# Performance work log

Hardware: AMD Instinct MI355X
Metric: run time of the kernel (lower is better)

## Reference

```python
import jax, jax.numpy as jnp
import numpy as np

EPS = 1e-5
H, I, E = 1024, 2048, 8


def _swiglu(x, wg, wu, wd):
    # x: [T,H], wg/wu: [H,I], wd: [I,H]
    return (jax.nn.silu(x @ wg) * (x @ wu)) @ wd


def setup_inputs() -> dict:
    key = jax.random.key(0)
    ks = jax.random.split(key, 12)
    B, S = 2, 2048
    s_h = 1.0 / np.sqrt(H)
    s_i = 1.0 / np.sqrt(I)
    return {
        "x": jax.random.normal(ks[0], (B, S, H), jnp.float32),
        "temporal_context": jax.random.normal(ks[1], (B, S, H), jnp.float32),
        "tp_w": jax.random.normal(ks[2], (H, H), jnp.float32) * s_h,
        "tp_b": jnp.zeros((H,), jnp.float32),
        "gate_w": jax.random.normal(ks[3], (H, E), jnp.float32) * 0.01,
        "eg": jax.random.normal(ks[4], (E, H, I), jnp.float32) * s_h,
        "eu": jax.random.normal(ks[5], (E, H, I), jnp.float32) * s_h,
        "ed": jax.random.normal(ks[6], (E, I, H), jnp.float32) * s_i,
        "sg": jax.random.normal(ks[7], (H, I), jnp.float32) * s_h,
        "su": jax.random.normal(ks[8], (H, I), jnp.float32) * s_h,
        "sd": jax.random.normal(ks[9], (I, H), jnp.float32) * s_i,
        "top_k": 2,
    }


def reference(x, temporal_context, tp_w, tp_b, gate_w, eg, eu, ed, sg, su, sd, top_k):
    B, S, Hd = x.shape
    xf = x.reshape(-1, Hd)                      # [T,H] tokens
    tc = temporal_context.reshape(-1, Hd)
    # Router: add temporal projection, softmax gate, top-k renormalized
    xr = xf + tc @ tp_w + tp_b
    probs = jax.nn.softmax(xr @ gate_w, axis=-1)            # [T,E]
    topk_p, topk_i = jax.lax.top_k(probs, top_k)            # [T,K]
    topk_p = topk_p / (topk_p.sum(-1, keepdims=True) + EPS)
    # Dense combine weights: combine[t,e] = sum_k topk_p[t,k] * 1[topk_i[t,k]==e]
    combine = jnp.einsum("tke,tk->te", jax.nn.one_hot(topk_i, E, dtype=x.dtype), topk_p)
    # Expert SwiGLU (grouped GEMM over all experts)
    h = jax.nn.silu(jnp.einsum("th,ehi->tei", xf, eg)) * jnp.einsum("th,ehi->tei", xf, eu)
    eout = jnp.einsum("tei,eih->teh", h, ed)                # [T,E,H]
    out = jnp.einsum("te,teh->th", combine, eout)
    # Shared expert applied to every token
    out = out + _swiglu(xf, sg, su, sd)
    return out.reshape(B, S, Hd)
```

## Files before the change

### kernel.cpp

```cpp
#include <hip/hip_runtime.h>
#include <hip/hip_bf16.h>
#include <stdint.h>

#define HDIM 1024
#define IDIM 2048
#define NEXP 8
#define NEXP1 9
#define TTOK 4096
#define REPS 1e-5f

typedef __bf16 bf16_t;
typedef __bf16 bf16x8 __attribute__((ext_vector_type(8)));
typedef __bf16 bf16x4 __attribute__((ext_vector_type(4)));
typedef float f32x4 __attribute__((ext_vector_type(4)));

__global__ __launch_bounds__(256) void k_convert(const float* __restrict__ src,
                                                 bf16_t* __restrict__ dst) {
    size_t i = ((size_t)blockIdx.x * 256 + threadIdx.x) * 4;
    float4 v = *(const float4*)(src + i);
    bf16x4 o = {(__bf16)v.x, (__bf16)v.y, (__bf16)v.z, (__bf16)v.w};
    *(bf16x4*)(dst + i) = o;
}

__global__ __launch_bounds__(256) void k_transpose(const float* __restrict__ src,
                                                   bf16_t* __restrict__ dst, int R, int C) {
    __shared__ float tile[32][33];
    size_t mat = (size_t)blockIdx.z * (size_t)R * (size_t)C;
    src += mat;
    dst += mat;
    int c0 = blockIdx.x * 32, r0 = blockIdx.y * 32;
    int tx = threadIdx.x, ty = threadIdx.y;
    for (int i = ty; i < 32; i += 8)
        tile[i][tx] = src[(size_t)(r0 + i) * C + c0 + tx];
    __syncthreads();
    for (int i = ty; i < 32; i += 8)
        dst[(size_t)(c0 + i) * R + r0 + tx] = (bf16_t)tile[tx][i];
}

__global__ __launch_bounds__(256) void k_router_prep(const float* __restrict__ tp_w,
                                                     const float* __restrict__ tp_b,
                                                     const float* __restrict__ gw,
                                                     float* __restrict__ A_r,
                                                     float* __restrict__ bg) {
    int idx = blockIdx.x * 256 + threadIdx.x;
    if (idx < HDIM * NEXP) {
        int h = idx >> 3, e = idx & 7;
        const float* wr = tp_w + (size_t)h * HDIM;
        float acc = 0.f;
        for (int j = 0; j < HDIM; j++) acc = fmaf(wr[j], gw[j * NEXP + e], acc);
        A_r[idx] = acc;
    } else if (idx < HDIM * NEXP + NEXP) {
        int e = idx - HDIM * NEXP;
        float acc = 0.f;
        for (int j = 0; j < HDIM; j++) acc = fmaf(tp_b[j], gw[j * NEXP + e], acc);
        bg[e] = acc;
    }
}

__global__ __launch_bounds__(256) void k_router(const float* __restrict__ x,
                                                const float* __restrict__ tcx,
                                                const float* __restrict__ gw,
                                                const float* __restrict__ A_r,
                                                const float* __restrict__ bg,
                                                int* __restrict__ cnt, int* __restrict__ tok,
                                                float* __restrict__ wl, int* __restrict__ sl) {
    int wave = threadIdx.x >> 6, lane = threadIdx.x & 63;
    int t = blockIdx.x * 4 + wave;
    const float* xr = x + (size_t)t * HDIM;
    const float* tr = tcx + (size_t)t * HDIM;
    float lg[NEXP];
    for (int e = 0; e < NEXP; e++) lg[e] = 0.f;
    for (int h = lane; h < HDIM; h += 64) {
        float xv = xr[h], tv = tr[h];
        const float4* g4 = (const float4*)(gw + h * NEXP);
        const float4* a4 = (const float4*)(A_r + h * NEXP);
        float4 g0 = g4[0], g1 = g4[1], a0 = a4[0], a1 = a4[1];
        lg[0] += xv * g0.x + tv * a0.x;
        lg[1] += xv * g0.y + tv * a0.y;
        lg[2] += xv * g0.z + tv * a0.z;
        lg[3] += xv * g0.w + tv * a0.w;
        lg[4] += xv * g1.x + tv * a1.x;
        lg[5] += xv * g1.y + tv * a1.y;
        lg[6] += xv * g1.z + tv * a1.z;
        lg[7] += xv * g1.w + tv * a1.w;
    }
    for (int off = 32; off > 0; off >>= 1)
        for (int e = 0; e < NEXP; e++) lg[e] += __shfl_xor(lg[e], off);
    if (lane == 0) {
        float m = -1e30f;
        for (int e = 0; e < NEXP; e++) {
            lg[e] += bg[e];
            m = fmaxf(m, lg[e]);
        }
        float p[NEXP], Z = 0.f;
        for (int e = 0; e < NEXP; e++) {
            p[e] = __expf(lg[e] - m);
            Z += p[e];
        }
        for (int e = 0; e < NEXP; e++) p[e] /= Z;
        int i1 = 0;
        float b1 = p[0];
        for (int e = 1; e < NEXP; e++)
            if (p[e] > b1) { b1 = p[e]; i1 = e; }
        int i2 = -1;
        float b2 = -1.f;
        for (int e = 0; e < NEXP; e++) {
            if (e == i1) continue;
            if (p[e] > b2) { b2 = p[e]; i2 = e; }
        }
        float s = b1 + b2 + REPS;
        float w1 = b1 / s, w2 = b2 / s;
        int p1 = atomicAdd(&cnt[i1], 1);
        tok[i1 * TTOK + p1] = t;
        wl[i1 * TTOK + p1] = w1;
        sl[i1 * TTOK + p1] = 2 * t;
        int p2 = atomicAdd(&cnt[i2], 1);
        tok[i2 * TTOK + p2] = t;
        wl[i2 * TTOK + p2] = w2;
        sl[i2 * TTOK + p2] = 2 * t + 1;
    }
}

__global__ __launch_bounds__(256) void k_fill_shared(int* __restrict__ cnt, int* __restrict__ tok,
                                                     float* __restrict__ wl, int* __restrict__ sl) {
    int t = blockIdx.x * 256 + threadIdx.x;
    tok[NEXP * TTOK + t] = t;
    wl[NEXP * TTOK + t] = 1.f;
    sl[NEXP * TTOK + t] = 2 * TTOK + t;
    if (t == 0) cnt[NEXP] = TTOK;
}

__global__ __launch_bounds__(256, 2) void k_gateup(const bf16_t* __restrict__ Xb,
                                                   const bf16_t* __restrict__ WgT,
                                                   const bf16_t* __restrict__ WuT,
                                                   bf16_t* __restrict__ Hout,
                                                   const int* __restrict__ tok_l,
                                                   const float* __restrict__ w_l,
                                                   const int* __restrict__ slot_l,
                                                   const int* __restrict__ cnt) {
    int e = blockIdx.z;
    int rows = cnt[e];
    int m0 = blockIdx.y * 128;
    if (m0 >= rows) return;
    int n0 = blockIdx.x * 64;
    const bf16_t* Wg = WgT + (size_t)e * IDIM * HDIM;
    const bf16_t* Wu = WuT + (size_t)e * IDIM * HDIM;
    const int* tl = tok_l + e * TTOK;
    const float* wlp = w_l + e * TTOK;
    const int* sl = slot_l + e * TTOK;

    __shared__ bf16_t As[128][72];
    __shared__ bf16_t Bg[64][72];
    __shared__ bf16_t Bu[64][72];

    int tid = threadIdx.x;
    int lane = tid & 63, wave = tid >> 6;
    int seg = tid & 7, rbase = tid >> 3;

    const bf16_t* aptr[4];
    for (int p = 0; p < 4; p++) {
        int g = m0 + p * 32 + rbase;
        int row = tl[min(g, rows - 1)];
        aptr[p] = Xb + (size_t)row * HDIM + seg * 8;
    }
    const bf16_t* gptr[2];
    const bf16_t* uptr[2];
    for (int p = 0; p < 2; p++) {
        int r = n0 + p * 32 + rbase;
        gptr[p] = Wg + (size_t)r * HDIM + seg * 8;
        uptr[p] = Wu + (size_t)r * HDIM + seg * 8;
    }

    f32x4 accg[2][4], accu[2][4];
    for (int a = 0; a < 2; a++)
        for (int b = 0; b < 4; b++) {
            accg[a][b] = (f32x4){0.f, 0.f, 0.f, 0.f};
            accu[a][b] = (f32x4){0.f, 0.f, 0.f, 0.f};
        }
    int lm = lane & 15, quad = lane >> 4;

    for (int k0 = 0; k0 < HDIM; k0 += 64) {
        for (int p = 0; p < 4; p++)
            *(bf16x8*)&As[p * 32 + rbase][seg * 8] = *(const bf16x8*)(aptr[p] + k0);
        for (int p = 0; p < 2; p++) {
            *(bf16x8*)&Bg[p * 32 + rbase][seg * 8] = *(const bf16x8*)(gptr[p] + k0);
            *(bf16x8*)&Bu[p * 32 + rbase][seg * 8] = *(const bf16x8*)(uptr[p] + k0);
        }
        __syncthreads();
        for (int kk = 0; kk < 2; kk++) {
            bf16x8 af[2], bgf[4], buf_[4];
            for (int mi = 0; mi < 2; mi++)
                af[mi] = *(const bf16x8*)&As[wave * 32 + mi * 16 + lm][kk * 32 + quad * 8];
            for (int ni = 0; ni < 4; ni++) {
                bgf[ni] = *(const bf16x8*)&Bg[ni * 16 + lm][kk * 32 + quad * 8];
                buf_[ni] = *(const bf16x8*)&Bu[ni * 16 + lm][kk * 32 + quad * 8];
            }
            for (int mi = 0; mi < 2; mi++)
                for (int ni = 0; ni < 4; ni++) {
                    accg[mi][ni] = __builtin_amdgcn_mfma_f32_16x16x32_bf16(af[mi], bgf[ni],
                                                                           accg[mi][ni], 0, 0, 0);
                    accu[mi][ni] = __builtin_amdgcn_mfma_f32_16x16x32_bf16(af[mi], buf_[ni],
                                                                           accu[mi][ni], 0, 0, 0);
                }
        }
        __syncthreads();
    }
    for (int mi = 0; mi < 2; mi++)
        for (int j = 0; j < 4; j++) {
            int r = m0 + wave * 32 + mi * 16 + quad * 4 + j;
            if (r >= rows) continue;
            int srow = sl[r];
            float w = wlp[r];
            bf16_t* hp = Hout + (size_t)srow * IDIM + n0 + lm;
            for (int ni = 0; ni < 4; ni++) {
                float g = accg[mi][ni][j];
                float u = accu[mi][ni][j];
                hp[ni * 16] = (bf16_t)(g / (1.f + __expf(-g)) * u * w);
            }
        }
}

__global__ __launch_bounds__(256, 2) void k_down(const bf16_t* __restrict__ Hin,
                                                 const bf16_t* __restrict__ WdT,
                                                 bf16_t* __restrict__ Eout,
                                                 const int* __restrict__ slot_l,
                                                 const int* __restrict__ cnt) {
    int e = blockIdx.z;
    int rows = cnt[e];
    int m0 = blockIdx.y * 128;
    if (m0 >= rows) return;
    int n0 = blockIdx.x * 128;
    const bf16_t* Wd = WdT + (size_t)e * HDIM * IDIM;
    const int* sl = slot_l + e * TTOK;

    __shared__ bf16_t As[128][72];
    __shared__ bf16_t Bs[128][72];

    int tid = threadIdx.x, lane = tid & 63, wave = tid >> 6;
    int seg = tid & 7, rbase = tid >> 3;
    const bf16_t* aptr[4];
    const bf16_t* bptr[4];
    for (int p = 0; p < 4; p++) {
        int g = m0 + p * 32 + rbase;
        int row = sl[min(g, rows - 1)];
        aptr[p] = Hin + (size_t)row * IDIM + seg * 8;
        bptr[p] = Wd + (size_t)(n0 + p * 32 + rbase) * IDIM + seg * 8;
    }
    f32x4 acc[4][4];
    for (int a = 0; a < 4; a++)
        for (int b = 0; b < 4; b++) acc[a][b] = (f32x4){0.f, 0.f, 0.f, 0.f};
    int wm = wave >> 1, wn = wave & 1;
    int lm = lane & 15, quad = lane >> 4;

    for (int k0 = 0; k0 < IDIM; k0 += 64) {
        for (int p = 0; p < 4; p++) {
            *(bf16x8*)&As[p * 32 + rbase][seg * 8] = *(const bf16x8*)(aptr[p] + k0);
            *(bf16x8*)&Bs[p * 32 + rbase][seg * 8] = *(const bf16x8*)(bptr[p] + k0);
        }
        __syncthreads();
        for (int kk = 0; kk < 2; kk++) {
            bf16x8 af[4], bf_[4];
            for (int mi = 0; mi < 4; mi++)
                af[mi] = *(const bf16x8*)&As[wm * 64 + mi * 16 + lm][kk * 32 + quad * 8];
            for (int ni = 0; ni < 4; ni++)
                bf_[ni] = *(const bf16x8*)&Bs[wn * 64 + ni * 16 + lm][kk * 32 + quad * 8];
            for (int mi = 0; mi < 4; mi++)
                for (int ni = 0; ni < 4; ni++)
                    acc[mi][ni] = __builtin_amdgcn_mfma_f32_16x16x32_bf16(af[mi], bf_[ni],
                                                                          acc[mi][ni], 0, 0, 0);
        }
        __syncthreads();
    }
    for (int mi = 0; mi < 4; mi++)
        for (int j = 0; j < 4; j++) {
            int r = m0 + wm * 64 + mi * 16 + quad * 4 + j;
            if (r >= rows) continue;
            int srow = sl[r];
            bf16_t* op = Eout + (size_t)srow * HDIM + n0 + wn * 64 + lm;
            for (int ni = 0; ni < 4; ni++) op[ni * 16] = (bf16_t)acc[mi][ni][j];
        }
}

__global__ __launch_bounds__(256) void k_combine(const bf16_t* __restrict__ Eout,
                                                 float* __restrict__ Out) {
    size_t i = ((size_t)blockIdx.x * 256 + threadIdx.x) * 8;
    size_t t = i / HDIM, h = i % HDIM;
    bf16x8 a = *(const bf16x8*)(Eout + (2 * t) * HDIM + h);
    bf16x8 b = *(const bf16x8*)(Eout + (2 * t + 1) * HDIM + h);
    bf16x8 c = *(const bf16x8*)(Eout + (size_t)(2 * TTOK + t) * HDIM + h);
    float* op = Out + i;
    for (int j = 0; j < 8; j++) op[j] = (float)a[j] + (float)b[j] + (float)c[j];
}

extern "C" void kernel_launch(void* const* d_in, const int* in_sizes, int n_in,
                              void* d_out, int out_size, void* d_ws, size_t ws_size,
                              hipStream_t stream) {
    const float* x = (const float*)d_in[0];
    const float* tcx = (const float*)d_in[1];
    const float* tp_w = (const float*)d_in[2];
    const float* tp_b = (const float*)d_in[3];
    const float* gate_w = (const float*)d_in[4];
    const float* eg = (const float*)d_in[5];
    const float* eu = (const float*)d_in[6];
    const float* ed = (const float*)d_in[7];
    const float* sg = (const float*)d_in[8];
    const float* su = (const float*)d_in[9];
    const float* sd = (const float*)d_in[10];
    float* out = (float*)d_out;

    char* wsp = (char*)d_ws;
    size_t off = 0;
    auto alloc = [&](size_t b) -> void* {
        void* p = wsp + off;
        off += (b + 255) & ~(size_t)255;
        return p;
    };
    bf16_t* xb = (bf16_t*)alloc((size_t)TTOK * HDIM * 2);
    bf16_t* WgT = (bf16_t*)alloc((size_t)NEXP1 * IDIM * HDIM * 2);
    bf16_t* WuT = (bf16_t*)alloc((size_t)NEXP1 * IDIM * HDIM * 2);
    bf16_t* WdT = (bf16_t*)alloc((size_t)NEXP1 * HDIM * IDIM * 2);
    float* A_r = (float*)alloc(HDIM * NEXP * 4);
    float* bg = (float*)alloc(NEXP * 4);
    int* cnt = (int*)alloc(NEXP1 * 4);
    int* tok = (int*)alloc(NEXP1 * TTOK * 4);
    float* wl = (float*)alloc(NEXP1 * TTOK * 4);
    int* sl = (int*)alloc(NEXP1 * TTOK * 4);
    bf16_t* hbuf = (bf16_t*)alloc((size_t)3 * TTOK * IDIM * 2);
    bf16_t* eout = (bf16_t*)alloc((size_t)3 * TTOK * HDIM * 2);

    hipMemsetAsync(cnt, 0, NEXP1 * 4, stream);
    k_convert<<<TTOK * HDIM / 1024, 256, 0, stream>>>(x, xb);
    dim3 tb(32, 8);
    k_transpose<<<dim3(IDIM / 32, HDIM / 32, NEXP), tb, 0, stream>>>(eg, WgT, HDIM, IDIM);
    k_transpose<<<dim3(IDIM / 32, HDIM / 32, NEXP), tb, 0, stream>>>(eu, WuT, HDIM, IDIM);
    k_transpose<<<dim3(HDIM / 32, IDIM / 32, NEXP), tb, 0, stream>>>(ed, WdT, IDIM, HDIM);
    k_transpose<<<dim3(IDIM / 32, HDIM / 32, 1), tb, 0, stream>>>(
        sg, WgT + (size_t)NEXP * IDIM * HDIM, HDIM, IDIM);
    k_transpose<<<dim3(IDIM / 32, HDIM / 32, 1), tb, 0, stream>>>(
        su, WuT + (size_t)NEXP * IDIM * HDIM, HDIM, IDIM);
    k_transpose<<<dim3(HDIM / 32, IDIM / 32, 1), tb, 0, stream>>>(
        sd, WdT + (size_t)NEXP * HDIM * IDIM, IDIM, HDIM);
    k_router_prep<<<33, 256, 0, stream>>>(tp_w, tp_b, gate_w, A_r, bg);
    k_router<<<TTOK / 4, 256, 0, stream>>>(x, tcx, gate_w, A_r, bg, cnt, tok, wl, sl);
    k_fill_shared<<<TTOK / 256, 256, 0, stream>>>(cnt, tok, wl, sl);
    k_gateup<<<dim3(IDIM / 64, TTOK / 128, NEXP1), 256, 0, stream>>>(xb, WgT, WuT, hbuf, tok, wl,
                                                                     sl, cnt);
    k_down<<<dim3(HDIM / 128, TTOK / 128, NEXP1), 256, 0, stream>>>(hbuf, WdT, eout, sl, cnt);
    k_combine<<<TTOK * HDIM / 2048, 256, 0, stream>>>(eout, out);
    (void)in_sizes; (void)n_in; (void)out_size; (void)ws_size;
}
```

Measured before the change: 720.0 us.

## Use direct global-to-LDS loads with XOR swizzle; widen weight transpose tiles

```diff
diff --git a/kernel.cpp b/kernel.cpp
--- a/kernel.cpp
+++ b/kernel.cpp
@@ -14,6 +14,12 @@
 typedef __bf16 bf16x4 __attribute__((ext_vector_type(4)));
 typedef float f32x4 __attribute__((ext_vector_type(4)));
 
+__device__ __forceinline__ void gl_lds16(const bf16_t* g, bf16_t* l) {
+    __builtin_amdgcn_global_load_lds(
+        (const __attribute__((address_space(1))) void*)g,
+        (__attribute__((address_space(3))) void*)l, 16, 0, 0);
+}
+
 __global__ __launch_bounds__(256) void k_convert(const float* __restrict__ src,
                                                  bf16_t* __restrict__ dst) {
     size_t i = ((size_t)blockIdx.x * 256 + threadIdx.x) * 4;
@@ -22,19 +28,27 @@
     *(bf16x4*)(dst + i) = o;
 }
 
-__global__ __launch_bounds__(256) void k_transpose(const float* __restrict__ src,
-                                                   bf16_t* __restrict__ dst, int R, int C) {
-    __shared__ float tile[32][33];
+__global__ __launch_bounds__(256) void k_transpose64(const float* __restrict__ src,
+                                                     bf16_t* __restrict__ dst, int R, int C) {
+    __shared__ float tile[64][65];
     size_t mat = (size_t)blockIdx.z * (size_t)R * (size_t)C;
-    src += mat;
-    dst += mat;
-    int c0 = blockIdx.x * 32, r0 = blockIdx.y * 32;
-    int tx = threadIdx.x, ty = threadIdx.y;
-    for (int i = ty; i < 32; i += 8)
-        tile[i][tx] = src[(size_t)(r0 + i) * C + c0 + tx];
+    int c0 = blockIdx.x * 64, r0 = blockIdx.y * 64;
+    int tid = threadIdx.x;
+    int rr = tid >> 4, cc = (tid & 15) * 4;
+    for (int i = 0; i < 4; i++) {
+        float4 v = *(const float4*)(src + mat + (size_t)(r0 + rr + i * 16) * C + c0 + cc);
+        tile[rr + i * 16][cc + 0] = v.x;
+        tile[rr + i * 16][cc + 1] = v.y;
+        tile[rr + i * 16][cc + 2] = v.z;
+        tile[rr + i * 16][cc + 3] = v.w;
+    }
     __syncthreads();
-    for (int i = ty; i < 32; i += 8)
-        dst[(size_t)(c0 + i) * R + r0 + tx] = (bf16_t)tile[tx][i];
+    int c = tid >> 2, s = (tid & 3) * 16;
+    bf16_t tmp[16];
+    for (int i = 0; i < 16; i++) tmp[i] = (bf16_t)tile[s + i][c];
+    bf16_t* op = dst + mat + (size_t)(c0 + c) * R + r0 + s;
+    *(bf16x8*)op = *(bf16x8*)tmp;
+    *(bf16x8*)(op + 8) = *(bf16x8*)(tmp + 8);
 }
 
 __global__ __launch_bounds__(256) void k_router_prep(const float* __restrict__ tp_w,
@@ -149,26 +163,27 @@
     const float* wlp = w_l + e * TTOK;
     const int* sl = slot_l + e * TTOK;
 
-    __shared__ bf16_t As[128][72];
-    __shared__ bf16_t Bg[64][72];
-    __shared__ bf16_t Bu[64][72];
+    __shared__ __align__(16) bf16_t As[128 * 64];
+    __shared__ __align__(16) bf16_t Bg[64 * 64];
+    __shared__ __align__(16) bf16_t Bu[64 * 64];
 
     int tid = threadIdx.x;
     int lane = tid & 63, wave = tid >> 6;
-    int seg = tid & 7, rbase = tid >> 3;
-
-    const bf16_t* aptr[4];
-    for (int p = 0; p < 4; p++) {
-        int g = m0 + p * 32 + rbase;
-        int row = tl[min(g, rows - 1)];
-        aptr[p] = Xb + (size_t)row * HDIM + seg * 8;
-    }
-    const bf16_t* gptr[2];
-    const bf16_t* uptr[2];
-    for (int p = 0; p < 2; p++) {
-        int r = n0 + p * 32 + rbase;
-        gptr[p] = Wg + (size_t)r * HDIM + seg * 8;
-        uptr[p] = Wu + (size_t)r * HDIM + seg * 8;
+    int lrow = lane >> 3;
+    int lchunk = (lane & 7) ^ lrow;
+
+    const bf16_t* asrc[4];
+    for (int j = 0; j < 4; j++) {
+        int r = (wave * 4 + j) * 8 + lrow;
+        int row = tl[min(m0 + r, rows - 1)];
+        asrc[j] = Xb + (size_t)row * HDIM + lchunk * 8;
+    }
+    const bf16_t* gsrc[2];
+    const bf16_t* usrc[2];
+    for (int j = 0; j < 2; j++) {
+        int r = (wave * 2 + j) * 8 + lrow;
+        gsrc[j] = Wg + (size_t)(n0 + r) * HDIM + lchunk * 8;
+        usrc[j] = Wu + (size_t)(n0 + r) * HDIM + lchunk * 8;
     }
 
     f32x4 accg[2][4], accu[2][4];
@@ -177,23 +192,23 @@
             accg[a][b] = (f32x4){0.f, 0.f, 0.f, 0.f};
             accu[a][b] = (f32x4){0.f, 0.f, 0.f, 0.f};
         }
-    int lm = lane & 15, quad = lane >> 4;
+    int lm = lane & 15, quad = lane >> 4, x7 = lm & 7;
 
     for (int k0 = 0; k0 < HDIM; k0 += 64) {
-        for (int p = 0; p < 4; p++)
-            *(bf16x8*)&As[p * 32 + rbase][seg * 8] = *(const bf16x8*)(aptr[p] + k0);
-        for (int p = 0; p < 2; p++) {
-            *(bf16x8*)&Bg[p * 32 + rbase][seg * 8] = *(const bf16x8*)(gptr[p] + k0);
-            *(bf16x8*)&Bu[p * 32 + rbase][seg * 8] = *(const bf16x8*)(uptr[p] + k0);
+        for (int j = 0; j < 4; j++) gl_lds16(asrc[j] + k0, As + (wave * 4 + j) * 512);
+        for (int j = 0; j < 2; j++) {
+            gl_lds16(gsrc[j] + k0, Bg + (wave * 2 + j) * 512);
+            gl_lds16(usrc[j] + k0, Bu + (wave * 2 + j) * 512);
         }
         __syncthreads();
         for (int kk = 0; kk < 2; kk++) {
+            int cg = ((kk * 4 + quad) ^ x7) * 8;
             bf16x8 af[2], bgf[4], buf_[4];
             for (int mi = 0; mi < 2; mi++)
-                af[mi] = *(const bf16x8*)&As[wave * 32 + mi * 16 + lm][kk * 32 + quad * 8];
+                af[mi] = *(const bf16x8*)&As[(wave * 32 + mi * 16 + lm) * 64 + cg];
             for (int ni = 0; ni < 4; ni++) {
-                bgf[ni] = *(const bf16x8*)&Bg[ni * 16 + lm][kk * 32 + quad * 8];
-                buf_[ni] = *(const bf16x8*)&Bu[ni * 16 + lm][kk * 32 + quad * 8];
+                bgf[ni] = *(const bf16x8*)&Bg[(ni * 16 + lm) * 64 + cg];
+                buf_[ni] = *(const bf16x8*)&Bu[(ni * 16 + lm) * 64 + cg];
             }
             for (int mi = 0; mi < 2; mi++)
                 for (int ni = 0; ni < 4; ni++) {
@@ -233,37 +248,40 @@
     const bf16_t* Wd = WdT + (size_t)e * HDIM * IDIM;
     const int* sl = slot_l + e * TTOK;
 
-    __shared__ bf16_t As[128][72];
-    __shared__ bf16_t Bs[128][72];
+    __shared__ __align__(16) bf16_t As[128 * 64];
+    __shared__ __align__(16) bf16_t Bs[128 * 64];
 
     int tid = threadIdx.x, lane = tid & 63, wave = tid >> 6;
-    int seg = tid & 7, rbase = tid >> 3;
-    const bf16_t* aptr[4];
-    const bf16_t* bptr[4];
-    for (int p = 0; p < 4; p++) {
-        int g = m0 + p * 32 + rbase;
-        int row = sl[min(g, rows - 1)];
-        aptr[p] = Hin + (size_t)row * IDIM + seg * 8;
-        bptr[p] = Wd + (size_t)(n0 + p * 32 + rbase) * IDIM + seg * 8;
+    int lrow = lane >> 3;
+    int lchunk = (lane & 7) ^ lrow;
+
+    const bf16_t* asrc[4];
+    const bf16_t* bsrc[4];
+    for (int j = 0; j < 4; j++) {
+        int r = (wave * 4 + j) * 8 + lrow;
+        int arow = sl[min(m0 + r, rows - 1)];
+        asrc[j] = Hin + (size_t)arow * IDIM + lchunk * 8;
+        bsrc[j] = Wd + (size_t)(n0 + r) * IDIM + lchunk * 8;
     }
     f32x4 acc[4][4];
     for (int a = 0; a < 4; a++)
         for (int b = 0; b < 4; b++) acc[a][b] = (f32x4){0.f, 0.f, 0.f, 0.f};
     int wm = wave >> 1, wn = wave & 1;
-    int lm = lane & 15, quad = lane >> 4;
+    int lm = lane & 15, quad = lane >> 4, x7 = lm & 7;
 
     for (int k0 = 0; k0 < IDIM; k0 += 64) {
-        for (int p = 0; p < 4; p++) {
-            *(bf16x8*)&As[p * 32 + rbase][seg * 8] = *(const bf16x8*)(aptr[p] + k0);
-            *(bf16x8*)&Bs[p * 32 + rbase][seg * 8] = *(const bf16x8*)(bptr[p] + k0);
+        for (int j = 0; j < 4; j++) {
+            gl_lds16(asrc[j] + k0, As + (wave * 4 + j) * 512);
+            gl_lds16(bsrc[j] + k0, Bs + (wave * 4 + j) * 512);
         }
         __syncthreads();
         for (int kk = 0; kk < 2; kk++) {
+            int cg = ((kk * 4 + quad) ^ x7) * 8;
             bf16x8 af[4], bf_[4];
             for (int mi = 0; mi < 4; mi++)
-                af[mi] = *(const bf16x8*)&As[wm * 64 + mi * 16 + lm][kk * 32 + quad * 8];
+                af[mi] = *(const bf16x8*)&As[(wm * 64 + mi * 16 + lm) * 64 + cg];
             for (int ni = 0; ni < 4; ni++)
-                bf_[ni] = *(const bf16x8*)&Bs[wn * 64 + ni * 16 + lm][kk * 32 + quad * 8];
+                bf_[ni] = *(const bf16x8*)&Bs[(wn * 64 + ni * 16 + lm) * 64 + cg];
             for (int mi = 0; mi < 4; mi++)
                 for (int ni = 0; ni < 4; ni++)
                     acc[mi][ni] = __builtin_amdgcn_mfma_f32_16x16x32_bf16(af[mi], bf_[ni],
@@ -330,15 +348,14 @@
 
     hipMemsetAsync(cnt, 0, NEXP1 * 4, stream);
     k_convert<<<TTOK * HDIM / 1024, 256, 0, stream>>>(x, xb);
-    dim3 tb(32, 8);
-    k_transpose<<<dim3(IDIM / 32, HDIM / 32, NEXP), tb, 0, stream>>>(eg, WgT, HDIM, IDIM);
-    k_transpose<<<dim3(IDIM / 32, HDIM / 32, NEXP), tb, 0, stream>>>(eu, WuT, HDIM, IDIM);
-    k_transpose<<<dim3(HDIM / 32, IDIM / 32, NEXP), tb, 0, stream>>>(ed, WdT, IDIM, HDIM);
-    k_transpose<<<dim3(IDIM / 32, HDIM / 32, 1), tb, 0, stream>>>(
+    k_transpose64<<<dim3(IDIM / 64, HDIM / 64, NEXP), 256, 0, stream>>>(eg, WgT, HDIM, IDIM);
+    k_transpose64<<<dim3(IDIM / 64, HDIM / 64, NEXP), 256, 0, stream>>>(eu, WuT, HDIM, IDIM);
+    k_transpose64<<<dim3(HDIM / 64, IDIM / 64, NEXP), 256, 0, stream>>>(ed, WdT, IDIM, HDIM);
+    k_transpose64<<<dim3(IDIM / 64, HDIM / 64, 1), 256, 0, stream>>>(
         sg, WgT + (size_t)NEXP * IDIM * HDIM, HDIM, IDIM);
-    k_transpose<<<dim3(IDIM / 32, HDIM / 32, 1), tb, 0, stream>>>(
+    k_transpose64<<<dim3(IDIM / 64, HDIM / 64, 1), 256, 0, stream>>>(
         su, WuT + (size_t)NEXP * IDIM * HDIM, HDIM, IDIM);
-    k_transpose<<<dim3(HDIM / 32, IDIM / 32, 1), tb, 0, stream>>>(
+    k_transpose64<<<dim3(HDIM / 64, IDIM / 64, 1), 256, 0, stream>>>(
         sd, WdT + (size_t)NEXP * HDIM * IDIM, IDIM, HDIM);
     k_router_prep<<<33, 256, 0, stream>>>(tp_w, tp_b, gate_w, A_r, bg);
     k_router<<<TTOK / 4, 256, 0, stream>>>(x, tcx, gate_w, A_r, bg, cnt, tok, wl, sl);
```

Measured after the change: 642.8 us. 10.7% less time.
